# Performance work log

Hardware: AMD Instinct MI355X
Metric: run time of the kernel (lower is better)

## Reference

```python
import jax, jax.numpy as jnp
import numpy as np
from jax.ops import segment_sum, segment_max

N, E, DS, DZ = 16384, 262144, 384, 128
H, D, PQ, PV = 12, 16, 4, 8
EPS = 1e-8


def _quat_to_rot(q):
    q = q / jnp.linalg.norm(q, axis=-1, keepdims=True)
    w, x, y, z = q[:, 0], q[:, 1], q[:, 2], q[:, 3]
    R = jnp.stack([
        1 - 2 * (y * y + z * z), 2 * (x * y - w * z), 2 * (x * z + w * y),
        2 * (x * y + w * z), 1 - 2 * (x * x + z * z), 2 * (y * z - w * x),
        2 * (x * z - w * y), 2 * (y * z + w * x), 1 - 2 * (x * x + y * y),
    ], axis=-1).reshape(-1, 3, 3)
    return R


def setup_inputs() -> dict:
    key = jax.random.key(0)
    ks = jax.random.split(key, 20)
    s = jax.random.normal(ks[0], (N, DS), jnp.float32)
    z = jax.random.normal(ks[1], (E, DZ), jnp.float32)
    edge_index = jax.random.randint(ks[2], (E, 2), 0, N, jnp.int64)
    # valid rigid frames: rotation from random unit quaternion + translation
    R = _quat_to_rot(jax.random.normal(ks[3], (N, 4), jnp.float32))
    t = jax.random.normal(ks[4], (N, 3), jnp.float32)
    f = jnp.zeros((N, 4, 4), jnp.float32).at[:, :3, :3].set(R)
    f = f.at[:, :3, 3].set(t).at[:, 3, 3].set(1.0)

    def lin(k, dout, din):
        return jax.random.normal(k, (dout, din), jnp.float32) / np.sqrt(din)

    hc, hpqk, hpv = H * D, H * PQ * 3, H * PV * 3
    s_out_dim = H * (D * 2 + PV * 4)
    params = dict(
        Wq=lin(ks[5], hc, DS), bq=jnp.zeros((hc,), jnp.float32),
        Wk=lin(ks[6], hc, DS), bk=jnp.zeros((hc,), jnp.float32),
        Wv=lin(ks[7], hc, DS), bv=jnp.zeros((hc,), jnp.float32),
        Wb=lin(ks[8], H, DZ), bb=jnp.zeros((H,), jnp.float32),
        Wqp=lin(ks[9], hpqk, DS), bqp=jnp.zeros((hpqk,), jnp.float32),
        Wkp=lin(ks[10], hpqk, DS), bkp=jnp.zeros((hpqk,), jnp.float32),
        Wvp=lin(ks[11], hpv, DS), bvp=jnp.zeros((hpv,), jnp.float32),
        head_weights=jnp.full((H,), 0.541324854612918, jnp.float32),
        Wpair=lin(ks[12], hc, DZ), bpair=jnp.zeros((hc,), jnp.float32),
        Wo=lin(ks[13], DS, s_out_dim), bo=jnp.zeros((DS,), jnp.float32),
    )
    return dict(s=s, z=z, f=f, edge_index=edge_index, **params)


def _ipa(s, z, f, edge_index, Wq, bq, Wk, bk, Wv, bv, Wb, bb,
         Wqp, bqp, Wkp, bkp, Wvp, bvp, head_weights, Wpair, bpair, Wo, bo):
    n = s.shape[0]
    R, t = f[:, :3, :3], f[:, :3, 3]
    idx_i, idx_j = edge_index[:, 0], edge_index[:, 1]

    norm_attn = (3.0 * D) ** 0.5          # (1/(3d))**-0.5 as in source
    norm_bias = 3.0 ** 0.5
    norm_pt = -0.5 * (3.0 * (PQ * 9.0 / 2)) ** 0.5

    q = (s @ Wq.T + bq).reshape(n, H, D)
    k = (s @ Wk.T + bk).reshape(n, H, D)
    v = (s @ Wv.T + bv).reshape(n, H, D)

    def to_global(pts):  # [n,H,P,3] local -> global
        return jnp.einsum('nij,nhpj->nhpi', R, pts) + t[:, None, None, :]

    q_pts = to_global((s @ Wqp.T + bqp).reshape(n, H, PQ, 3))
    k_pts = to_global((s @ Wkp.T + bkp).reshape(n, H, PQ, 3))
    v_pts = to_global((s @ Wvp.T + bvp).reshape(n, H, PV, 3))

    # scalar QK term + learned pair bias, per edge [E,H]
    attn = jnp.einsum('ehd,ehd->eh', q[idx_i], k[idx_j]) * norm_attn
    attn = attn + (z @ Wb.T + bb) * norm_bias
    # point-distance term
    diff = q_pts[idx_i] - k_pts[idx_j]            # [E,H,PQ,3]
    pt_att = (diff ** 2).sum((-1, -2))            # [E,H]
    pt_att = pt_att * (jax.nn.softplus(head_weights) * norm_pt)
    attn = attn + pt_att

    # segment softmax over edges grouped by destination node idx_i
    m = segment_max(attn, idx_i, num_segments=n)          # [N,H]
    ex = jnp.exp(attn - m[idx_i])
    denom = segment_sum(ex, idx_i, num_segments=n)
    a = ex / denom[idx_i]                                  # [E,H]

    o = segment_sum(a[:, :, None] * v[idx_j], idx_i, num_segments=n)  # [N,H,D]
    o = o.reshape(n, H * D)

    o_pts_g = segment_sum(a[:, :, None, None] * v_pts[idx_j], idx_i,
                          num_segments=n)                  # [N,H,PV,3]
    o_pts_g = o_pts_g.reshape(n, H * PV, 3)
    # invert_apply: R^T (p - t)
    o_pts = jnp.einsum('nji,npj->npi', R, o_pts_g - t[:, None, :])
    o_pts_norm = jnp.sqrt((o_pts ** 2).sum(-1) + EPS)      # [N,H*PV]
    o_pts_flat = o_pts.reshape(n, H * PV * 3)

    v_pair = (z @ Wpair.T + bpair).reshape(-1, H, D)       # [E,H,D]
    o_pair = segment_sum(a[:, :, None] * v_pair, idx_i, num_segments=n)
    o_pair = o_pair.reshape(n, H * D)

    o_s = jnp.concatenate([o, o_pts_flat, o_pts_norm, o_pair], axis=-1)
    return o_s @ Wo.T + bo


def reference(s, z, f, edge_index, Wq, bq, Wk, bk, Wv, bv, Wb, bb,
              Wqp, bqp, Wkp, bkp, Wvp, bvp, head_weights, Wpair, bpair, Wo, bo):
    s_out = _ipa(s, z, f, edge_index, Wq, bq, Wk, bk, Wv, bv, Wb, bb,
                 Wqp, bqp, Wkp, bkp, Wvp, bvp, head_weights, Wpair, bpair, Wo, bo)
    return (s_out, z)
```

## Files before the change

kernel.cpp:

```cpp
#include <hip/hip_runtime.h>

#define NNODE 16384
#define NEDGE 262144
#define DS    384
#define DZ    128
#define NH    12
#define HD    16
#define HC    192
#define HPQK  144
#define HPV   288
#define NCAT  1152
#define FEAT  2144
#define SOUT  384

typedef _Float16 f16;
typedef _Float16 f16x8 __attribute__((ext_vector_type(8)));
typedef _Float16 f16x4 __attribute__((ext_vector_type(4)));
typedef _Float16 f16x2 __attribute__((ext_vector_type(2)));
typedef float    f32x4v __attribute__((ext_vector_type(4)));

#define AS3(p) ((__attribute__((address_space(3))) void*)(p))
#define AS1(p) ((const __attribute__((address_space(1))) void*)(p))
#define WAVE_LDS_FENCE() asm volatile("s_waitcnt lgkmcnt(0)" ::: "memory")

__global__ void k_prep(const float* __restrict__ Wq, const float* __restrict__ Wk,
                       const float* __restrict__ Wv, const float* __restrict__ Wqp,
                       const float* __restrict__ Wkp, const float* __restrict__ Wvp,
                       const float* __restrict__ bq, const float* __restrict__ bk,
                       const float* __restrict__ bv, const float* __restrict__ bqp,
                       const float* __restrict__ bkp, const float* __restrict__ bvp,
                       const float* __restrict__ Wb, const float* __restrict__ Wo,
                       const float* __restrict__ Wpair, const float* __restrict__ bpair,
                       const float* __restrict__ hw,
                       f16* __restrict__ Wcat, float* __restrict__ bcat,
                       f16* __restrict__ Wb16, f16* __restrict__ M2,
                       float* __restrict__ gamv)
{
    int t = blockIdx.x * 256 + threadIdx.x;
    const int T0 = NCAT * DS;
    const int T1 = T0 + NCAT;
    const int T2 = T1 + 16 * DZ;
    const int T3 = T2 + SOUT * FEAT;
    const int T4 = T3 + NH;
    if (t < T0) {
        int r = t / DS, c = t - r * DS;
        float v;
        if      (r < 192) v = Wq [(r      ) * DS + c];
        else if (r < 384) v = Wk [(r - 192) * DS + c];
        else if (r < 576) v = Wv [(r - 384) * DS + c];
        else if (r < 720) v = Wqp[(r - 576) * DS + c];
        else if (r < 864) v = Wkp[(r - 720) * DS + c];
        else              v = Wvp[(r - 864) * DS + c];
        Wcat[t] = (f16)v;
    } else if (t < T1) {
        int r = t - T0;
        float v;
        if      (r < 192) v = bq [r];
        else if (r < 384) v = bk [r - 192];
        else if (r < 576) v = bv [r - 384];
        else if (r < 720) v = bqp[r - 576];
        else if (r < 864) v = bkp[r - 720];
        else              v = bvp[r - 864];
        bcat[r] = v;
    } else if (t < T2) {
        int q = t - T1;
        Wb16[q] = (q < NH * DZ) ? (f16)Wb[q] : (f16)0.0f;
    } else if (t < T3) {
        int q = t - T2;
        int r = q / FEAT, c = q - r * FEAT;
        float v = 0.f;
        if (c < 576) {
            v = Wo[r * 768 + c];
        } else if (c < 2112) {
            int h = (c - 576) >> 7, cc = (c - 576) & 127;
            float acc = 0.f;
            #pragma unroll
            for (int d = 0; d < 16; ++d)
                acc += Wo[r * 768 + 576 + h * 16 + d] * Wpair[(h * 16 + d) * DZ + cc];
            v = acc;
        } else if (c < 2124) {
            int h = c - 2112;
            float acc = 0.f;
            #pragma unroll
            for (int d = 0; d < 16; ++d)
                acc += Wo[r * 768 + 576 + h * 16 + d] * bpair[h * 16 + d];
            v = acc;
        }
        M2[q] = (f16)v;
    } else if (t < T4) {
        int h = t - T3;
        gamv[h] = -3.67423461f * log1pf(__expf(hw[h]));
    }
}

__global__ void k_convert_s(const float4* __restrict__ s4, f16* __restrict__ s16)
{
    int t = blockIdx.x * 256 + threadIdx.x;
    float4 v = s4[t];
    f16x4 o = { (f16)v.x, (f16)v.y, (f16)v.z, (f16)v.w };
    *(f16x4*)(s16 + 4 * (size_t)t) = o;
}

__global__ void k_convert_z(const float* __restrict__ z, const int* __restrict__ inv,
                            f16* __restrict__ z16s)
{
    int t = blockIdx.x * 256 + threadIdx.x;
    int e = t >> 1, half = t & 1;
    int pos = inv[e];
    const float4* zr = (const float4*)(z + (size_t)e * DZ + half * 64);
    f16* zo = z16s + (size_t)pos * DZ + half * 64;
    #pragma unroll
    for (int c = 0; c < 16; ++c) {
        float4 v = zr[c];
        f16x4 o = { (f16)v.x, (f16)v.y, (f16)v.z, (f16)v.w };
        *(f16x4*)(zo + 4 * c) = o;
    }
}

__global__ __launch_bounds__(256) void k_zbias(const f16* __restrict__ z16s,
                                               const f16* __restrict__ Wb16,
                                               const float* __restrict__ bb,
                                               float* __restrict__ zbias)
{
    const int wv = threadIdx.x >> 6, lane = threadIdx.x & 63;
    const int row0 = (blockIdx.x * 4 + wv) * 64;
    f16x8 bf[4];
    #pragma unroll
    for (int ks = 0; ks < 4; ++ks)
        bf[ks] = *(const f16x8*)(Wb16 + (lane & 15) * DZ + ks * 32 + (lane >> 4) * 8);
    #pragma unroll
    for (int tt = 0; tt < 4; ++tt) {
        int ra = row0 + tt * 16 + (lane & 15);
        f32x4v acc = {};
        #pragma unroll
        for (int ks = 0; ks < 4; ++ks) {
            f16x8 af = *(const f16x8*)(z16s + (size_t)ra * DZ + ks * 32 + (lane >> 4) * 8);
            acc = __builtin_amdgcn_mfma_f32_16x16x32_f16(af, bf[ks], acc, 0, 0, 0);
        }
        int col = lane & 15;
        if (col < NH) {
            #pragma unroll
            for (int r = 0; r < 4; ++r) {
                int row = row0 + tt * 16 + (lane >> 4) * 4 + r;
                zbias[(size_t)row * NH + col] = (acc[r] + bb[col]) * 1.73205081f;
            }
        }
    }
}

__global__ __launch_bounds__(256) void k_gemm(const f16* __restrict__ A, const f16* __restrict__ B,
                                              const float* __restrict__ bias, float* __restrict__ C,
                                              int M, int N, int K)
{
    __shared__ __align__(16) f16 As[128 * 32];
    __shared__ __align__(16) f16 Bs[128 * 32];
    const int tid = threadIdx.x;
    const int wave = tid >> 6, lane = tid & 63;
    const int bm = blockIdx.x, bn = blockIdx.y;
    const int wm = (wave >> 1) * 64, wn = (wave & 1) * 64;
    f32x4v acc[4][4] = {};
    const int srow = wave * 16 + (lane >> 2);
    const int scol = (lane & 3) * 8;
    const f16* gA0 = A + (size_t)(bm * 128 + srow) * K + scol;
    const f16* gA1 = A + (size_t)(bm * 128 + srow + 64) * K + scol;
    const f16* gB0 = B + (size_t)(bn * 128 + srow) * K + scol;
    const f16* gB1 = B + (size_t)(bn * 128 + srow + 64) * K + scol;
    f16* lA0 = As + wave * 512;
    f16* lA1 = As + (wave + 4) * 512;
    f16* lB0 = Bs + wave * 512;
    f16* lB1 = Bs + (wave + 4) * 512;
    const int fr = lane & 15, fc = (lane >> 4) * 8;
    const int nK = K >> 5;
    for (int kk = 0; kk < nK; ++kk) {
        __syncthreads();
        __builtin_amdgcn_global_load_lds(AS1(gA0), AS3(lA0), 16, 0, 0);
        __builtin_amdgcn_global_load_lds(AS1(gA1), AS3(lA1), 16, 0, 0);
        __builtin_amdgcn_global_load_lds(AS1(gB0), AS3(lB0), 16, 0, 0);
        __builtin_amdgcn_global_load_lds(AS1(gB1), AS3(lB1), 16, 0, 0);
        gA0 += 32; gA1 += 32; gB0 += 32; gB1 += 32;
        __syncthreads();
        f16x8 af[4], bf[4];
        #pragma unroll
        for (int mi = 0; mi < 4; ++mi)
            af[mi] = *(const f16x8*)(As + (wm + mi * 16 + fr) * 32 + fc);
        #pragma unroll
        for (int ni = 0; ni < 4; ++ni)
            bf[ni] = *(const f16x8*)(Bs + (wn + ni * 16 + fr) * 32 + fc);
        #pragma unroll
        for (int mi = 0; mi < 4; ++mi)
            #pragma unroll
            for (int ni = 0; ni < 4; ++ni)
                acc[mi][ni] = __builtin_amdgcn_mfma_f32_16x16x32_f16(af[mi], bf[ni], acc[mi][ni], 0, 0, 0);
    }
    const int r0 = bm * 128 + wm + (lane >> 4) * 4;
    const int c0 = bn * 128 + wn + (lane & 15);
    #pragma unroll
    for (int mi = 0; mi < 4; ++mi)
        #pragma unroll
        for (int ni = 0; ni < 4; ++ni) {
            int col = c0 + ni * 16;
            float b = bias[col];
            #pragma unroll
            for (int r = 0; r < 4; ++r) {
                int row = r0 + mi * 16 + r;
                C[(size_t)row * N + col] = acc[mi][ni][r] + b;
            }
        }
}

__global__ __launch_bounds__(256) void k_gemm16(const f16* __restrict__ A, const f16* __restrict__ B,
                                                const float* __restrict__ bias, f16* __restrict__ C,
                                                int M, int N, int K)
{
    __shared__ __align__(16) f16 As[128 * 32];
    __shared__ __align__(16) f16 Bs[128 * 32];
    const int tid = threadIdx.x;
    const int wave = tid >> 6, lane = tid & 63;
    const int bm = blockIdx.x, bn = blockIdx.y;
    const int wm = (wave >> 1) * 64, wn = (wave & 1) * 64;
    f32x4v acc[4][4] = {};
    const int srow = wave * 16 + (lane >> 2);
    const int scol = (lane & 3) * 8;
    const f16* gA0 = A + (size_t)(bm * 128 + srow) * K + scol;
    const f16* gA1 = A + (size_t)(bm * 128 + srow + 64) * K + scol;
    const f16* gB0 = B + (size_t)(bn * 128 + srow) * K + scol;
    const f16* gB1 = B + (size_t)(bn * 128 + srow + 64) * K + scol;
    f16* lA0 = As + wave * 512;
    f16* lA1 = As + (wave + 4) * 512;
    f16* lB0 = Bs + wave * 512;
    f16* lB1 = Bs + (wave + 4) * 512;
    const int fr = lane & 15, fc = (lane >> 4) * 8;
    const int nK = K >> 5;
    for (int kk = 0; kk < nK; ++kk) {
        __syncthreads();
        __builtin_amdgcn_global_load_lds(AS1(gA0), AS3(lA0), 16, 0, 0);
        __builtin_amdgcn_global_load_lds(AS1(gA1), AS3(lA1), 16, 0, 0);
        __builtin_amdgcn_global_load_lds(AS1(gB0), AS3(lB0), 16, 0, 0);
        __builtin_amdgcn_global_load_lds(AS1(gB1), AS3(lB1), 16, 0, 0);
        gA0 += 32; gA1 += 32; gB0 += 32; gB1 += 32;
        __syncthreads();
        f16x8 af[4], bf[4];
        #pragma unroll
        for (int mi = 0; mi < 4; ++mi)
            af[mi] = *(const f16x8*)(As + (wm + mi * 16 + fr) * 32 + fc);
        #pragma unroll
        for (int ni = 0; ni < 4; ++ni)
            bf[ni] = *(const f16x8*)(Bs + (wn + ni * 16 + fr) * 32 + fc);
        #pragma unroll
        for (int mi = 0; mi < 4; ++mi)
            #pragma unroll
            for (int ni = 0; ni < 4; ++ni)
                acc[mi][ni] = __builtin_amdgcn_mfma_f32_16x16x32_f16(af[mi], bf[ni], acc[mi][ni], 0, 0, 0);
    }
    const int r0 = bm * 128 + wm + (lane >> 4) * 4;
    const int c0 = bn * 128 + wn + (lane & 15);
    #pragma unroll
    for (int mi = 0; mi < 4; ++mi)
        #pragma unroll
        for (int ni = 0; ni < 4; ++ni) {
            int col = c0 + ni * 16;
            float b = bias[col];
            #pragma unroll
            for (int r = 0; r < 4; ++r) {
                int row = r0 + mi * 16 + r;
                C[(size_t)row * N + col] = (f16)(acc[mi][ni][r] + b);
            }
        }
}

__global__ __launch_bounds__(64) void k_nodepost(const f16* __restrict__ raw, const float* __restrict__ fmat,
        f16* __restrict__ Q16, f16* __restrict__ K16, f16* __restrict__ V16,
        f16* __restrict__ QP16, f16* __restrict__ KP16, f16* __restrict__ VP16)
{
    int n = blockIdx.x, l = threadIdx.x;
    const f16* r = raw + (size_t)n * NCAT;
    #pragma unroll
    for (int q = 0; q < 3; ++q) {
        int c = q * 64 + l;
        Q16[(size_t)n * HC + c] = r[c];
        K16[(size_t)n * HC + c] = r[HC + c];
        V16[(size_t)n * HC + c] = r[2 * HC + c];
    }
    const float* fp = fmat + (size_t)n * 16;
    float R00 = fp[0], R01 = fp[1], R02 = fp[2],  t0 = fp[3];
    float R10 = fp[4], R11 = fp[5], R12 = fp[6],  t1 = fp[7];
    float R20 = fp[8], R21 = fp[9], R22 = fp[10], t2 = fp[11];
    if (l < 48) {
        const f16* p = r + 576 + 3 * l;
        float x = (float)p[0], y = (float)p[1], zz = (float)p[2];
        QP16[(size_t)n * HPQK + 3 * l + 0] = (f16)(R00 * x + R01 * y + R02 * zz + t0);
        QP16[(size_t)n * HPQK + 3 * l + 1] = (f16)(R10 * x + R11 * y + R12 * zz + t1);
        QP16[(size_t)n * HPQK + 3 * l + 2] = (f16)(R20 * x + R21 * y + R22 * zz + t2);
        const f16* p2 = r + 720 + 3 * l;
        float x2 = (float)p2[0], y2 = (float)p2[1], z2 = (float)p2[2];
        KP16[(size_t)n * HPQK + 3 * l + 0] = (f16)(R00 * x2 + R01 * y2 + R02 * z2 + t0);
        KP16[(size_t)n * HPQK + 3 * l + 1] = (f16)(R10 * x2 + R11 * y2 + R12 * z2 + t1);
        KP16[(size_t)n * HPQK + 3 * l + 2] = (f16)(R20 * x2 + R21 * y2 + R22 * z2 + t2);
    }
    {
        const f16* p = r + 864 + 3 * l;
        float x = (float)p[0], y = (float)p[1], zz = (float)p[2];
        VP16[(size_t)n * HPV + 3 * l + 0] = (f16)(R00 * x + R01 * y + R02 * zz + t0);
        VP16[(size_t)n * HPV + 3 * l + 1] = (f16)(R10 * x + R11 * y + R12 * zz + t1);
        VP16[(size_t)n * HPV + 3 * l + 2] = (f16)(R20 * x + R21 * y + R22 * zz + t2);
    }
    if (l < 32) {
        int tt = 64 + l;
        const f16* p = r + 864 + 3 * tt;
        float x = (float)p[0], y = (float)p[1], zz = (float)p[2];
        VP16[(size_t)n * HPV + 3 * tt + 0] = (f16)(R00 * x + R01 * y + R02 * zz + t0);
        VP16[(size_t)n * HPV + 3 * tt + 1] = (f16)(R10 * x + R11 * y + R12 * zz + t1);
        VP16[(size_t)n * HPV + 3 * tt + 2] = (f16)(R20 * x + R21 * y + R22 * zz + t2);
    }
}

__global__ void k_zero(int* counts, int* cursor) {
    int t = blockIdx.x * 256 + threadIdx.x;
    if (t < NNODE) counts[t] = 0;
    else if (t < 2 * NNODE) cursor[t - NNODE] = 0;
}
__global__ void k_count(const int* __restrict__ ei, int* counts) {
    int e = blockIdx.x * 256 + threadIdx.x;
    if (e < NEDGE) atomicAdd(&counts[ei[2 * e]], 1);
}
__global__ void k_scan(const int* __restrict__ counts, int* __restrict__ rowptr) {
    __shared__ int lds[256];
    int t = threadIdx.x;
    const int per = NNODE / 256;
    int s = 0;
    for (int i = 0; i < per; ++i) s += counts[t * per + i];
    lds[t] = s; __syncthreads();
    for (int off = 1; off < 256; off <<= 1) {
        int v = (t >= off) ? lds[t - off] : 0;
        __syncthreads();
        lds[t] += v;
        __syncthreads();
    }
    int run = (t == 0) ? 0 : lds[t - 1];
    for (int i = 0; i < per; ++i) { rowptr[t * per + i] = run; run += counts[t * per + i]; }
    if (t == 255) rowptr[NNODE] = run;
}
__global__ void k_scatter(const int* __restrict__ ei, const int* __restrict__ rowptr,
                          int* cursor, int* __restrict__ inv, int* __restrict__ jsorted,
                          int* __restrict__ isorted) {
    int e = blockIdx.x * 256 + threadIdx.x;
    if (e < NEDGE) {
        int i = ei[2 * e];
        int pos = rowptr[i] + atomicAdd(&cursor[i], 1);
        inv[e] = pos;
        jsorted[pos] = ei[2 * e + 1];
        isorted[pos] = i;
    }
}

__global__ __launch_bounds__(256) void k_logits2(
    const int* __restrict__ isorted, const int* __restrict__ jsorted,
    const float* __restrict__ zbias,
    const f16* __restrict__ Q16, const f16* __restrict__ K16,
    const f16* __restrict__ QP16, const f16* __restrict__ KP16,
    const float* __restrict__ gamv, float* __restrict__ attn)
{
    const int pos = blockIdx.x * 256 + threadIdx.x;
    const int i = isorted[pos], j = jsorted[pos];
    const f16x8* qr = (const f16x8*)(Q16 + (size_t)i * HC);
    const f16x8* kr = (const f16x8*)(K16 + (size_t)j * HC);
    const f16* qpp = QP16 + (size_t)i * HPQK;
    const f16* kpp = KP16 + (size_t)j * HPQK;
    const float4* zbp = (const float4*)(zbias + (size_t)pos * NH);
    float4 zb0 = zbp[0], zb1 = zbp[1], zb2 = zbp[2];
    float zb[NH] = { zb0.x, zb0.y, zb0.z, zb0.w, zb1.x, zb1.y, zb1.z, zb1.w,
                     zb2.x, zb2.y, zb2.z, zb2.w };
    float out[NH];
    #pragma unroll
    for (int h = 0; h < NH; ++h) {
        f16x8 q0 = qr[2 * h], q1 = qr[2 * h + 1];
        f16x8 k0 = kr[2 * h], k1 = kr[2 * h + 1];
        float d = 0.f;
        #pragma unroll
        for (int u = 0; u < 8; ++u)
            d += (float)q0[u] * (float)k0[u] + (float)q1[u] * (float)k1[u];
        float pt = 0.f;
        #pragma unroll
        for (int c = 0; c < 3; ++c) {
            f16x4 qpc = *(const f16x4*)(qpp + 12 * h + 4 * c);
            f16x4 kpc = *(const f16x4*)(kpp + 12 * h + 4 * c);
            #pragma unroll
            for (int u = 0; u < 4; ++u) {
                float dd = (float)qpc[u] - (float)kpc[u];
                pt += dd * dd;
            }
        }
        out[h] = 6.92820323f * d + zb[h] + gamv[h] * pt;
    }
    float4* ao = (float4*)(attn + (size_t)pos * NH);
    ao[0] = make_float4(out[0], out[1], out[2], out[3]);
    ao[1] = make_float4(out[4], out[5], out[6], out[7]);
    ao[2] = make_float4(out[8], out[9], out[10], out[11]);
}

__global__ __launch_bounds__(256) void k_soft(
    const int* __restrict__ rowptr, const float* __restrict__ attn,
    f16* __restrict__ a16, f16* __restrict__ feat)
{
    const int lane = threadIdx.x & 63, wv = threadIdx.x >> 6;
    const int slot = lane >> 4, el = lane & 15;
    const int n = blockIdx.x * 16 + wv * 4 + slot;
    const int base = rowptr[n], deg = rowptr[n + 1] - base;

    f16* fo = feat + (size_t)n * FEAT;
    fo[2112 + el]      = (f16)((el < NH && deg > 0) ? 1.0f : 0.0f);
    fo[2112 + 16 + el] = (f16)0.0f;

    float lg[NH];
    if (deg <= 16) {
        if (el < deg) {
            const float4* ar = (const float4*)(attn + (size_t)(base + el) * NH);
            float4 a0 = ar[0], a1 = ar[1], a2 = ar[2];
            lg[0]=a0.x; lg[1]=a0.y; lg[2]=a0.z; lg[3]=a0.w;
            lg[4]=a1.x; lg[5]=a1.y; lg[6]=a1.z; lg[7]=a1.w;
            lg[8]=a2.x; lg[9]=a2.y; lg[10]=a2.z; lg[11]=a2.w;
        } else {
            #pragma unroll
            for (int h = 0; h < NH; ++h) lg[h] = -1e30f;
        }
        #pragma unroll
        for (int h = 0; h < NH; ++h) {
            float v = lg[h];
            v = fmaxf(v, __shfl_xor(v, 1));
            v = fmaxf(v, __shfl_xor(v, 2));
            v = fmaxf(v, __shfl_xor(v, 4));
            v = fmaxf(v, __shfl_xor(v, 8));
            float e = __expf(lg[h] - v);
            float ssum = e;
            ssum += __shfl_xor(ssum, 1);
            ssum += __shfl_xor(ssum, 2);
            ssum += __shfl_xor(ssum, 4);
            ssum += __shfl_xor(ssum, 8);
            lg[h] = (ssum > 0.f) ? e / ssum : 0.f;
        }
        if (el < deg) {
            f16x8 o0, o1;
            #pragma unroll
            for (int h = 0; h < 8; ++h) o0[h] = (f16)lg[h];
            #pragma unroll
            for (int h = 8; h < 12; ++h) o1[h - 8] = (f16)lg[h];
            o1[4] = o1[5] = o1[6] = o1[7] = (f16)0.0f;
            f16* ap = a16 + (size_t)(base + el) * 16;
            *(f16x8*)ap = o0;
            *(f16x8*)(ap + 8) = o1;
        }
    } else {
        const int nch = (deg + 15) >> 4;
        float mx[NH];
        #pragma unroll
        for (int h = 0; h < NH; ++h) mx[h] = -1e30f;
        for (int c = 0; c < nch; ++c) {
            int idx = c * 16 + el;
            if (idx < deg) {
                const float4* ar = (const float4*)(attn + (size_t)(base + idx) * NH);
                float4 a0 = ar[0], a1 = ar[1], a2 = ar[2];
                float v[NH] = { a0.x,a0.y,a0.z,a0.w, a1.x,a1.y,a1.z,a1.w, a2.x,a2.y,a2.z,a2.w };
                #pragma unroll
                for (int h = 0; h < NH; ++h) mx[h] = fmaxf(mx[h], v[h]);
            }
        }
        #pragma unroll
        for (int h = 0; h < NH; ++h) {
            float v = mx[h];
            v = fmaxf(v, __shfl_xor(v, 1));
            v = fmaxf(v, __shfl_xor(v, 2));
            v = fmaxf(v, __shfl_xor(v, 4));
            v = fmaxf(v, __shfl_xor(v, 8));
            mx[h] = v;
        }
        float ls[NH] = {};
        for (int c = 0; c < nch; ++c) {
            int idx = c * 16 + el;
            if (idx < deg) {
                const float4* ar = (const float4*)(attn + (size_t)(base + idx) * NH);
                float4 a0 = ar[0], a1 = ar[1], a2 = ar[2];
                float v[NH] = { a0.x,a0.y,a0.z,a0.w, a1.x,a1.y,a1.z,a1.w, a2.x,a2.y,a2.z,a2.w };
                f16x8 o0, o1;
                #pragma unroll
                for (int h = 0; h < NH; ++h) {
                    float e = __expf(v[h] - mx[h]);
                    ls[h] += e;
                    if (h < 8) o0[h] = (f16)e; else o1[h - 8] = (f16)e;
                }
                o1[4] = o1[5] = o1[6] = o1[7] = (f16)0.0f;
                f16* ap = a16 + (size_t)(base + idx) * 16;
                *(f16x8*)ap = o0;
                *(f16x8*)(ap + 8) = o1;
            }
        }
        float il[NH];
        #pragma unroll
        for (int h = 0; h < NH; ++h) {
            float v = ls[h];
            v += __shfl_xor(v, 1);
            v += __shfl_xor(v, 2);
            v += __shfl_xor(v, 4);
            v += __shfl_xor(v, 8);
            il[h] = (v > 0.f) ? 1.0f / v : 0.f;
        }
        for (int c = 0; c < nch; ++c) {
            int idx = c * 16 + el;
            if (idx < deg) {
                f16* ap = a16 + (size_t)(base + idx) * 16;
                f16x8 o0 = *(f16x8*)ap;
                f16x8 o1 = *(f16x8*)(ap + 8);
                #pragma unroll
                for (int h = 0; h < 8; ++h) o0[h] = (f16)((float)o0[h] * il[h]);
                #pragma unroll
                for (int h = 8; h < 12; ++h) o1[h - 8] = (f16)((float)o1[h - 8] * il[h]);
                *(f16x8*)ap = o0;
                *(f16x8*)(ap + 8) = o1;
            }
        }
    }
}

__global__ __launch_bounds__(256) void k_aggu(
    const int* __restrict__ rowptr, const f16* __restrict__ a16,
    const f16* __restrict__ z16s, f16* __restrict__ feat)
{
    __shared__ f16 ash[4][64 * 16];
    const int wv = threadIdx.x >> 6, lane = threadIdx.x & 63;
    const int n = blockIdx.x * 4 + wv;
    const int base = rowptr[n], deg = rowptr[n + 1] - base;
    float u0[NH] = {}, u1[NH] = {};
    const int nch = (deg + 63) >> 6;
    for (int c = 0; c < nch; ++c) {
        int cl = min(64, deg - c * 64);
        if (lane < cl) {
            const f16x8* ap = (const f16x8*)(a16 + (size_t)(base + c * 64 + lane) * 16);
            *(f16x8*)&ash[wv][lane * 16] = ap[0];
            *(f16x8*)&ash[wv][lane * 16 + 8] = ap[1];
        }
        WAVE_LDS_FENCE();
        for (int kk = 0; kk < cl; ++kk) {
            size_t pos = (size_t)(base + c * 64 + kk);
            f16x2 zv = *(const f16x2*)(z16s + pos * DZ + 2 * lane);
            float z0 = (float)zv[0], z1 = (float)zv[1];
            #pragma unroll
            for (int i = 0; i < 6; ++i) {
                f16x2 a2 = *(const f16x2*)&ash[wv][kk * 16 + 2 * i];
                float a0 = (float)a2[0], a1 = (float)a2[1];
                u0[2 * i]     += a0 * z0; u1[2 * i]     += a0 * z1;
                u0[2 * i + 1] += a1 * z0; u1[2 * i + 1] += a1 * z1;
            }
        }
        WAVE_LDS_FENCE();
    }
    f16* fo = feat + (size_t)n * FEAT + 576;
    #pragma unroll
    for (int h = 0; h < NH; ++h) {
        f16x2 o = { (f16)u0[h], (f16)u1[h] };
        *(f16x2*)(fo + h * DZ + 2 * lane) = o;
    }
}

__global__ __launch_bounds__(256) void k_aggv(
    const int* __restrict__ rowptr, const int* __restrict__ jsorted,
    const f16* __restrict__ a16, const f16* __restrict__ V16,
    const f16* __restrict__ VP16, const float* __restrict__ fmat,
    f16* __restrict__ feat)
{
    __shared__ f16 ash[4][64 * 16];
    __shared__ int jsh[4][64];
    __shared__ float psh[2][HPV];
    const int w4 = threadIdx.x >> 6;
    const int lane = threadIdx.x & 63;
    const int slot = w4 >> 1;
    const int role = w4 & 1;
    const int n = blockIdx.x * 2 + slot;
    const int base = rowptr[n], deg = rowptr[n + 1] - base;
    const int nch = (deg + 63) >> 6;

    float o0 = 0, o1 = 0, o2 = 0;
    const int hA = lane >> 4, hB = (64 + lane) >> 4, hC2 = (128 + lane) >> 4;
    float acc[5] = {};
    int hk[5];
    #pragma unroll
    for (int k = 0; k < 5; ++k) hk[k] = (k * 64 + lane) / 24;

    for (int c = 0; c < nch; ++c) {
        int cl = min(64, deg - c * 64);
        if (lane < cl) {
            size_t pos = (size_t)(base + c * 64 + lane);
            const f16x8* ap = (const f16x8*)(a16 + pos * 16);
            *(f16x8*)&ash[w4][lane * 16] = ap[0];
            *(f16x8*)&ash[w4][lane * 16 + 8] = ap[1];
            jsh[w4][lane] = jsorted[pos];
        }
        WAVE_LDS_FENCE();
        if (role == 0) {
            for (int kk = 0; kk < cl; ++kk) {
                int j = jsh[w4][kk];
                const f16* vr = V16 + (size_t)j * HC;
                float aA = (float)ash[w4][kk * 16 + hA];
                float aB = (float)ash[w4][kk * 16 + hB];
                float aC = (float)ash[w4][kk * 16 + hC2];
                o0 += aA * (float)vr[lane];
                o1 += aB * (float)vr[64 + lane];
                o2 += aC * (float)vr[128 + lane];
            }
        } else {
            for (int kk = 0; kk < cl; ++kk) {
                int j = jsh[w4][kk];
                const f16* vp = VP16 + (size_t)j * HPV;
                #pragma unroll
                for (int k = 0; k < 4; ++k)
                    acc[k] += (float)ash[w4][kk * 16 + hk[k]] * (float)vp[k * 64 + lane];
                if (lane < 32)
                    acc[4] += (float)ash[w4][kk * 16 + hk[4]] * (float)vp[256 + lane];
            }
        }
        WAVE_LDS_FENCE();
    }

    f16* fo = feat + (size_t)n * FEAT;
    if (role == 0) {
        fo[lane] = (f16)o0; fo[64 + lane] = (f16)o1; fo[128 + lane] = (f16)o2;
    } else {
        #pragma unroll
        for (int k = 0; k < 4; ++k) psh[slot][k * 64 + lane] = acc[k];
        if (lane < 32) psh[slot][256 + lane] = acc[4];
        WAVE_LDS_FENCE();
        const float* fp = fmat + (size_t)n * 16;
        float R00 = fp[0], R01 = fp[1], R02 = fp[2],  t0 = fp[3];
        float R10 = fp[4], R11 = fp[5], R12 = fp[6],  t1 = fp[7];
        float R20 = fp[8], R21 = fp[9], R22 = fp[10], t2 = fp[11];
        {
            int P = lane;
            float gx = psh[slot][3 * P] - t0, gy = psh[slot][3 * P + 1] - t1, gz = psh[slot][3 * P + 2] - t2;
            float lx = R00 * gx + R10 * gy + R20 * gz;
            float ly = R01 * gx + R11 * gy + R21 * gz;
            float lz = R02 * gx + R12 * gy + R22 * gz;
            fo[192 + 3 * P] = (f16)lx; fo[192 + 3 * P + 1] = (f16)ly; fo[192 + 3 * P + 2] = (f16)lz;
            fo[480 + P] = (f16)sqrtf(lx * lx + ly * ly + lz * lz + 1e-8f);
        }
        if (lane < 32) {
            int P = 64 + lane;
            float gx = psh[slot][3 * P] - t0, gy = psh[slot][3 * P + 1] - t1, gz = psh[slot][3 * P + 2] - t2;
            float lx = R00 * gx + R10 * gy + R20 * gz;
            float ly = R01 * gx + R11 * gy + R21 * gz;
            float lz = R02 * gx + R12 * gy + R22 * gz;
            fo[192 + 3 * P] = (f16)lx; fo[192 + 3 * P + 1] = (f16)ly; fo[192 + 3 * P + 2] = (f16)lz;
            fo[480 + P] = (f16)sqrtf(lx * lx + ly * ly + lz * lz + 1e-8f);
        }
    }
}

extern "C" void kernel_launch(void* const* d_in, const int* in_sizes, int n_in,
                              void* d_out, int out_size, void* d_ws, size_t ws_size,
                              hipStream_t stream)
{
    (void)in_sizes; (void)n_in; (void)out_size; (void)ws_size;
    const float* s     = (const float*)d_in[0];
    const float* z     = (const float*)d_in[1];
    const float* fmat  = (const float*)d_in[2];
    const int*   ei    = (const int*)d_in[3];
    const float* Wq    = (const float*)d_in[4];
    const float* bq    = (const float*)d_in[5];
    const float* Wk    = (const float*)d_in[6];
    const float* bk    = (const float*)d_in[7];
    const float* Wv    = (const float*)d_in[8];
    const float* bv    = (const float*)d_in[9];
    const float* Wb    = (const float*)d_in[10];
    const float* bb    = (const float*)d_in[11];
    const float* Wqp   = (const float*)d_in[12];
    const float* bqp   = (const float*)d_in[13];
    const float* Wkp   = (const float*)d_in[14];
    const float* bkp   = (const float*)d_in[15];
    const float* Wvp   = (const float*)d_in[16];
    const float* bvp   = (const float*)d_in[17];
    const float* hw    = (const float*)d_in[18];
    const float* Wpair = (const float*)d_in[19];
    const float* bpair = (const float*)d_in[20];
    const float* Wo    = (const float*)d_in[21];
    const float* bo    = (const float*)d_in[22];

    char* w = (char*)d_ws;
    auto alloc = [&](size_t bytes) { char* p = w; w += (bytes + 255) & ~(size_t)255; return p; };
    f16*   s16     = (f16*)  alloc((size_t)NNODE * DS * 2);
    f16*   Wcat    = (f16*)  alloc((size_t)NCAT * DS * 2);
    float* bcat    = (float*)alloc((size_t)NCAT * 4);
    f16*   Wb16    = (f16*)  alloc((size_t)16 * DZ * 2);
    f16*   M2      = (f16*)  alloc((size_t)SOUT * FEAT * 2);
    float* gamv    = (float*)alloc((size_t)NH * 4);
    int*   counts  = (int*)  alloc((size_t)NNODE * 4);
    int*   rowptr  = (int*)  alloc((size_t)(NNODE + 1) * 4);
    int*   cursor  = (int*)  alloc((size_t)NNODE * 4);
    int*   inv     = (int*)  alloc((size_t)NEDGE * 4);
    int*   jsorted = (int*)  alloc((size_t)NEDGE * 4);
    int*   isorted = (int*)  alloc((size_t)NEDGE * 4);
    float* attn    = (float*)alloc((size_t)NEDGE * NH * 4);
    f16*   z16s    = (f16*)  alloc((size_t)NEDGE * DZ * 2);
    float* zbias   = (float*)alloc((size_t)NEDGE * NH * 4);
    f16*   Q16     = (f16*)  alloc((size_t)NNODE * HC * 2);
    f16*   K16     = (f16*)  alloc((size_t)NNODE * HC * 2);
    f16*   QP16    = (f16*)  alloc((size_t)NNODE * HPQK * 2);
    f16*   KP16    = (f16*)  alloc((size_t)NNODE * HPQK * 2);
    f16*   V16     = (f16*)  alloc((size_t)NNODE * HC * 2);
    f16*   VP16    = (f16*)  alloc((size_t)NNODE * HPV * 2);
    f16*   a16     = (f16*)  alloc((size_t)NEDGE * 16 * 2);
    char*  U       = w;
    f16*   raw16   = (f16*)U;
    f16*   feat    = (f16*)U;

    float* zout = (float*)d_out + (size_t)NNODE * DS;

    hipMemcpyAsync(zout, z, (size_t)NEDGE * DZ * 4, hipMemcpyDeviceToDevice, stream);

    const int PREP_T = NCAT * DS + NCAT + 16 * DZ + SOUT * FEAT + NH;
    k_prep<<<(PREP_T + 255) / 256, 256, 0, stream>>>(Wq, Wk, Wv, Wqp, Wkp, Wvp,
        bq, bk, bv, bqp, bkp, bvp, Wb, Wo, Wpair, bpair, hw, Wcat, bcat, Wb16, M2, gamv);
    k_zero<<<(2 * NNODE) / 256, 256, 0, stream>>>(counts, cursor);
    k_count<<<NEDGE / 256, 256, 0, stream>>>(ei, counts);
    k_scan<<<1, 256, 0, stream>>>(counts, rowptr);
    k_scatter<<<NEDGE / 256, 256, 0, stream>>>(ei, rowptr, cursor, inv, jsorted, isorted);
    k_convert_s<<<(NNODE * DS / 4) / 256, 256, 0, stream>>>((const float4*)s, s16);
    k_convert_z<<<(NEDGE * 2) / 256, 256, 0, stream>>>(z, inv, z16s);
    k_zbias<<<NEDGE / 256, 256, 0, stream>>>(z16s, Wb16, bb, zbias);
    k_gemm16<<<dim3(NNODE / 128, NCAT / 128), 256, 0, stream>>>(s16, Wcat, bcat, raw16,
        NNODE, NCAT, DS);
    k_nodepost<<<NNODE, 64, 0, stream>>>(raw16, fmat, Q16, K16, V16, QP16, KP16, VP16);
    k_logits2<<<NEDGE / 256, 256, 0, stream>>>(isorted, jsorted, zbias, Q16, K16,
        QP16, KP16, gamv, attn);
    k_soft<<<NNODE / 16, 256, 0, stream>>>(rowptr, attn, a16, feat);
    k_aggu<<<NNODE / 4, 256, 0, stream>>>(rowptr, a16, z16s, feat);
    k_aggv<<<NNODE / 2, 256, 0, stream>>>(rowptr, jsorted, a16, V16, VP16, fmat, feat);
    k_gemm<<<dim3(NNODE / 128, SOUT / 128), 256, 0, stream>>>(feat, M2, bo, (float*)d_out,
        NNODE, SOUT, FEAT);
}
```

Before: 440.6 us.

## Fuse z passthrough copy with fp16 conversion and gather z by edge id

```diff
diff --git a/kernel.cpp b/kernel.cpp
--- a/kernel.cpp
+++ b/kernel.cpp
@@ -101,23 +101,17 @@
     *(f16x4*)(s16 + 4 * (size_t)t) = o;
 }
 
-__global__ void k_convert_z(const float* __restrict__ z, const int* __restrict__ inv,
-                            f16* __restrict__ z16s)
+__global__ void k_zcopy(const float4* __restrict__ z4, f16* __restrict__ z16,
+                        float4* __restrict__ zout4)
 {
     int t = blockIdx.x * 256 + threadIdx.x;
-    int e = t >> 1, half = t & 1;
-    int pos = inv[e];
-    const float4* zr = (const float4*)(z + (size_t)e * DZ + half * 64);
-    f16* zo = z16s + (size_t)pos * DZ + half * 64;
-    #pragma unroll
-    for (int c = 0; c < 16; ++c) {
-        float4 v = zr[c];
-        f16x4 o = { (f16)v.x, (f16)v.y, (f16)v.z, (f16)v.w };
-        *(f16x4*)(zo + 4 * c) = o;
-    }
-}
-
-__global__ __launch_bounds__(256) void k_zbias(const f16* __restrict__ z16s,
+    float4 v = z4[t];
+    zout4[t] = v;
+    f16x4 o = { (f16)v.x, (f16)v.y, (f16)v.z, (f16)v.w };
+    *(f16x4*)(z16 + 4 * (size_t)t) = o;
+}
+
+__global__ __launch_bounds__(256) void k_zbias(const f16* __restrict__ z16,
                                                const f16* __restrict__ Wb16,
                                                const float* __restrict__ bb,
                                                float* __restrict__ zbias)
@@ -134,7 +128,7 @@
         f32x4v acc = {};
         #pragma unroll
         for (int ks = 0; ks < 4; ++ks) {
-            f16x8 af = *(const f16x8*)(z16s + (size_t)ra * DZ + ks * 32 + (lane >> 4) * 8);
+            f16x8 af = *(const f16x8*)(z16 + (size_t)ra * DZ + ks * 32 + (lane >> 4) * 8);
             acc = __builtin_amdgcn_mfma_f32_16x16x32_f16(af, bf[ks], acc, 0, 0, 0);
         }
         int col = lane & 15;
@@ -341,19 +335,20 @@
     if (t == 255) rowptr[NNODE] = run;
 }
 __global__ void k_scatter(const int* __restrict__ ei, const int* __restrict__ rowptr,
-                          int* cursor, int* __restrict__ inv, int* __restrict__ jsorted,
+                          int* cursor, int* __restrict__ eids, int* __restrict__ jsorted,
                           int* __restrict__ isorted) {
     int e = blockIdx.x * 256 + threadIdx.x;
     if (e < NEDGE) {
         int i = ei[2 * e];
         int pos = rowptr[i] + atomicAdd(&cursor[i], 1);
-        inv[e] = pos;
+        eids[pos] = e;
         jsorted[pos] = ei[2 * e + 1];
         isorted[pos] = i;
     }
 }
 
 __global__ __launch_bounds__(256) void k_logits2(
+    const int* __restrict__ eids,
     const int* __restrict__ isorted, const int* __restrict__ jsorted,
     const float* __restrict__ zbias,
     const f16* __restrict__ Q16, const f16* __restrict__ K16,
@@ -362,11 +357,12 @@
 {
     const int pos = blockIdx.x * 256 + threadIdx.x;
     const int i = isorted[pos], j = jsorted[pos];
+    const int e = eids[pos];
     const f16x8* qr = (const f16x8*)(Q16 + (size_t)i * HC);
     const f16x8* kr = (const f16x8*)(K16 + (size_t)j * HC);
     const f16* qpp = QP16 + (size_t)i * HPQK;
     const f16* kpp = KP16 + (size_t)j * HPQK;
-    const float4* zbp = (const float4*)(zbias + (size_t)pos * NH);
+    const float4* zbp = (const float4*)(zbias + (size_t)e * NH);
     float4 zb0 = zbp[0], zb1 = zbp[1], zb2 = zbp[2];
     float zb[NH] = { zb0.x, zb0.y, zb0.z, zb0.w, zb1.x, zb1.y, zb1.z, zb1.w,
                      zb2.x, zb2.y, zb2.z, zb2.w };
@@ -521,10 +517,11 @@
 }
 
 __global__ __launch_bounds__(256) void k_aggu(
-    const int* __restrict__ rowptr, const f16* __restrict__ a16,
-    const f16* __restrict__ z16s, f16* __restrict__ feat)
+    const int* __restrict__ rowptr, const int* __restrict__ eids,
+    const f16* __restrict__ a16, const f16* __restrict__ z16, f16* __restrict__ feat)
 {
     __shared__ f16 ash[4][64 * 16];
+    __shared__ int esh[4][64];
     const int wv = threadIdx.x >> 6, lane = threadIdx.x & 63;
     const int n = blockIdx.x * 4 + wv;
     const int base = rowptr[n], deg = rowptr[n + 1] - base;
@@ -533,14 +530,16 @@
     for (int c = 0; c < nch; ++c) {
         int cl = min(64, deg - c * 64);
         if (lane < cl) {
-            const f16x8* ap = (const f16x8*)(a16 + (size_t)(base + c * 64 + lane) * 16);
+            size_t pos = (size_t)(base + c * 64 + lane);
+            const f16x8* ap = (const f16x8*)(a16 + pos * 16);
             *(f16x8*)&ash[wv][lane * 16] = ap[0];
             *(f16x8*)&ash[wv][lane * 16 + 8] = ap[1];
+            esh[wv][lane] = eids[pos];
         }
         WAVE_LDS_FENCE();
         for (int kk = 0; kk < cl; ++kk) {
-            size_t pos = (size_t)(base + c * 64 + kk);
-            f16x2 zv = *(const f16x2*)(z16s + pos * DZ + 2 * lane);
+            int e = esh[wv][kk];
+            f16x2 zv = *(const f16x2*)(z16 + (size_t)e * DZ + 2 * lane);
             float z0 = (float)zv[0], z1 = (float)zv[1];
             #pragma unroll
             for (int i = 0; i < 6; ++i) {
@@ -692,11 +691,11 @@
     int*   counts  = (int*)  alloc((size_t)NNODE * 4);
     int*   rowptr  = (int*)  alloc((size_t)(NNODE + 1) * 4);
     int*   cursor  = (int*)  alloc((size_t)NNODE * 4);
-    int*   inv     = (int*)  alloc((size_t)NEDGE * 4);
+    int*   eids    = (int*)  alloc((size_t)NEDGE * 4);
     int*   jsorted = (int*)  alloc((size_t)NEDGE * 4);
     int*   isorted = (int*)  alloc((size_t)NEDGE * 4);
     float* attn    = (float*)alloc((size_t)NEDGE * NH * 4);
-    f16*   z16s    = (f16*)  alloc((size_t)NEDGE * DZ * 2);
+    f16*   z16     = (f16*)  alloc((size_t)NEDGE * DZ * 2);
     float* zbias   = (float*)alloc((size_t)NEDGE * NH * 4);
     f16*   Q16     = (f16*)  alloc((size_t)NNODE * HC * 2);
     f16*   K16     = (f16*)  alloc((size_t)NNODE * HC * 2);
@@ -711,25 +710,23 @@
 
     float* zout = (float*)d_out + (size_t)NNODE * DS;
 
-    hipMemcpyAsync(zout, z, (size_t)NEDGE * DZ * 4, hipMemcpyDeviceToDevice, stream);
-
     const int PREP_T = NCAT * DS + NCAT + 16 * DZ + SOUT * FEAT + NH;
     k_prep<<<(PREP_T + 255) / 256, 256, 0, stream>>>(Wq, Wk, Wv, Wqp, Wkp, Wvp,
         bq, bk, bv, bqp, bkp, bvp, Wb, Wo, Wpair, bpair, hw, Wcat, bcat, Wb16, M2, gamv);
     k_zero<<<(2 * NNODE) / 256, 256, 0, stream>>>(counts, cursor);
     k_count<<<NEDGE / 256, 256, 0, stream>>>(ei, counts);
     k_scan<<<1, 256, 0, stream>>>(counts, rowptr);
-    k_scatter<<<NEDGE / 256, 256, 0, stream>>>(ei, rowptr, cursor, inv, jsorted, isorted);
+    k_scatter<<<NEDGE / 256, 256, 0, stream>>>(ei, rowptr, cursor, eids, jsorted, isorted);
     k_convert_s<<<(NNODE * DS / 4) / 256, 256, 0, stream>>>((const float4*)s, s16);
-    k_convert_z<<<(NEDGE * 2) / 256, 256, 0, stream>>>(z, inv, z16s);
-    k_zbias<<<NEDGE / 256, 256, 0, stream>>>(z16s, Wb16, bb, zbias);
+    k_zcopy<<<(NEDGE * DZ / 4) / 256, 256, 0, stream>>>((const float4*)z, z16, (float4*)zout);
+    k_zbias<<<NEDGE / 256, 256, 0, stream>>>(z16, Wb16, bb, zbias);
     k_gemm16<<<dim3(NNODE / 128, NCAT / 128), 256, 0, stream>>>(s16, Wcat, bcat, raw16,
         NNODE, NCAT, DS);
     k_nodepost<<<NNODE, 64, 0, stream>>>(raw16, fmat, Q16, K16, V16, QP16, KP16, VP16);
-    k_logits2<<<NEDGE / 256, 256, 0, stream>>>(isorted, jsorted, zbias, Q16, K16,
+    k_logits2<<<NEDGE / 256, 256, 0, stream>>>(eids, isorted, jsorted, zbias, Q16, K16,
         QP16, KP16, gamv, attn);
     k_soft<<<NNODE / 16, 256, 0, stream>>>(rowptr, attn, a16, feat);
-    k_aggu<<<NNODE / 4, 256, 0, stream>>>(rowptr, a16, z16s, feat);
+    k_aggu<<<NNODE / 4, 256, 0, stream>>>(rowptr, eids, a16, z16, feat);
     k_aggv<<<NNODE / 2, 256, 0, stream>>>(rowptr, jsorted, a16, V16, VP16, fmat, feat);
     k_gemm<<<dim3(NNODE / 128, SOUT / 128), 256, 0, stream>>>(feat, M2, bo, (float*)d_out,
         NNODE, SOUT, FEAT);
```

Result: faster. 404.8 us (-8.1%).
